# Performance work log

Hardware: AMD Instinct MI355X
Metric: run time of the kernel (lower is better)

The kernel has to match this reference:

```python
import jax, jax.numpy as jnp
import numpy as np

BINS = 10

def setup_inputs() -> dict:
    key = jax.random.key(0)
    k1, k2 = jax.random.split(key)
    N, C = 262144, 80
    pred = jax.random.normal(k1, (N, C), dtype=jnp.float32)
    target = jax.random.randint(k2, (N, C), 0, 2, dtype=jnp.int32)
    return {"pred": pred, "target": target}


def _ghmc_loss(pred, target):
    # NOTE: faithful to the original torch code, which applies sigmoid to pred
    # and then feeds that *through binary_cross_entropy_with_logits* (i.e. the
    # sigmoid output is treated as logits -- a double sigmoid quirk we preserve).
    z = jax.nn.sigmoid(pred)                      # [N, C] "logits" fed to BCE-with-logits
    t = target.astype(z.dtype)                    # [N, C]
    # gradient magnitude, detached like pred.detach() in torch
    g = jnp.abs(jax.lax.stop_gradient(z) - t)     # in [0, 1]
    # label_weight is overwritten with ones in the original forward, so every
    # element is valid: tot = N * C.
    tot = jnp.asarray(z.size, dtype=z.dtype)

    # uniform bins: edges[i] = i/BINS, last edge nudged by 1e-6 so g == 1 lands
    # in the last bin -> equivalent to floor(g*BINS) clipped to BINS-1.
    idx = jnp.clip((g * BINS).astype(jnp.int32), 0, BINS - 1)   # [N, C]
    counts = jax.ops.segment_sum(
        jnp.ones((z.size,), dtype=z.dtype), idx.reshape(-1), num_segments=BINS
    )                                                            # [BINS]
    n_nonempty = jnp.sum(counts > 0).astype(z.dtype)
    per_bin_w = jnp.where(counts > 0, tot / jnp.maximum(counts, 1.0), 0.0)  # [BINS]
    weights = per_bin_w[idx] / jnp.maximum(n_nonempty, 1.0)      # [N, C]
    weights = jax.lax.stop_gradient(weights)

    # BCE-with-logits(z, t) = softplus(z) - t*z (numerically stable)
    bce = jax.nn.softplus(z) - t * z
    return jnp.sum(weights * bce) / tot


def reference(pred, target):
    return _ghmc_loss(pred, target)
```

## Files before the change

kernel.cpp:

```cpp
#include <hip/hip_runtime.h>


#define NBINS  10
#define GRID1  2048
#define BLOCK1 256

typedef float vf4 __attribute__((ext_vector_type(4)));
typedef int   vi4 __attribute__((ext_vector_type(4)));

#if __has_builtin(__builtin_amdgcn_exp2f)
__device__ __forceinline__ float nexp2(float a) { return __builtin_amdgcn_exp2f(a); }
#else
__device__ __forceinline__ float nexp2(float a) { return __expf(a * 0.69314718055994531f); }
#endif
#if __has_builtin(__builtin_amdgcn_logf)
__device__ __forceinline__ float nlog2(float a) { return __builtin_amdgcn_logf(a); }
#else
__device__ __forceinline__ float nlog2(float a) { return __logf(a) * 1.44269504088896341f; }
#endif

#define LOG2E 1.44269504088896341f
#define LN2   0.69314718055994531f

__global__ __launch_bounds__(BLOCK1) void ghmc_pass1(
    const vf4* __restrict__ pred4,
    const vi4* __restrict__ targ4,
    float* __restrict__ partial_s,
    int*   __restrict__ partial_c,
    int nvec4)
{
    __shared__ float sred[BLOCK1 / 64][NBINS];
    __shared__ int   cred[BLOCK1 / 64][NBINS];

    float s[NBINS];
#pragma unroll
    for (int b = 0; b < NBINS; ++b) s[b] = 0.0f;
    unsigned long long cnt = 0;

    const int idx    = blockIdx.x * BLOCK1 + threadIdx.x;
    const int stride = GRID1 * BLOCK1;

    auto group8 = [&](vf4 p0, vi4 t0, vf4 p1, vi4 t1) {
        float x[8], tf[8];
#pragma unroll
        for (int j = 0; j < 4; ++j) {
            x[j]     = p0[j];  tf[j]     = (float)t0[j];
            x[4 + j] = p1[j];  tf[4 + j] = (float)t1[j];
        }
        float z[8];
#pragma unroll
        for (int j = 0; j < 8; ++j)
            z[j] = __builtin_amdgcn_rcpf(1.0f + nexp2(-x[j] * LOG2E));
        asm volatile("" : "+v"(z[0]), "+v"(z[1]), "+v"(z[2]), "+v"(z[3]),
                         "+v"(z[4]), "+v"(z[5]), "+v"(z[6]), "+v"(z[7]));
        int bi[8]; float bce[8];
#pragma unroll
        for (int j = 0; j < 8; ++j) {
            float g = fabsf(z[j] - tf[j]);
            int   b = (int)(g * 10.0f);
            bi[j]   = b > (NBINS - 1) ? (NBINS - 1) : b;
            float sp = nlog2(1.0f + nexp2(z[j] * LOG2E)) * LN2;
            bce[j]  = sp - tf[j] * z[j];
        }
#pragma unroll
        for (int j = 0; j < 8; ++j) {
#pragma unroll
            for (int b = 0; b < NBINS; ++b)
                s[b] += (bi[j] == b) ? bce[j] : 0.0f;
            cnt += 1ull << (6 * bi[j]);
        }
    };

    int i = idx;
    for (; i + 3 * stride < nvec4; i += 4 * stride) {
        vf4 p0 = pred4[i];
        vi4 t0 = targ4[i];
        vf4 p1 = pred4[i + stride];
        vi4 t1 = targ4[i + stride];
        vf4 p2 = pred4[i + 2 * stride];
        vi4 t2 = targ4[i + 2 * stride];
        vf4 p3 = pred4[i + 3 * stride];
        vi4 t3 = targ4[i + 3 * stride];
        asm volatile("" : "+v"(p0), "+v"(t0), "+v"(p1), "+v"(t1),
                          "+v"(p2), "+v"(t2), "+v"(p3), "+v"(t3));
        group8(p0, t0, p1, t1);
        group8(p2, t2, p3, t3);
    }
    for (; i + stride < nvec4; i += 2 * stride) {
        vf4 p0 = pred4[i];
        vi4 t0 = targ4[i];
        vf4 p1 = pred4[i + stride];
        vi4 t1 = targ4[i + stride];
        asm volatile("" : "+v"(p0), "+v"(t0), "+v"(p1), "+v"(t1));
        group8(p0, t0, p1, t1);
    }
    if (i < nvec4) {
        vf4 p0 = pred4[i];
        vi4 t0 = targ4[i];
#pragma unroll
        for (int j = 0; j < 4; ++j) {
            float tfj = (float)t0[j];
            float zj  = __builtin_amdgcn_rcpf(1.0f + nexp2(-p0[j] * LOG2E));
            float g   = fabsf(zj - tfj);
            int   b   = (int)(g * 10.0f);
            b = b > (NBINS - 1) ? (NBINS - 1) : b;
            float bc  = nlog2(1.0f + nexp2(zj * LOG2E)) * LN2 - tfj * zj;
#pragma unroll
            for (int bb = 0; bb < NBINS; ++bb)
                s[bb] += (b == bb) ? bc : 0.0f;
            cnt += 1ull << (6 * b);
        }
    }

    int c[NBINS];
#pragma unroll
    for (int b = 0; b < NBINS; ++b) c[b] = (int)((cnt >> (6 * b)) & 63ull);

#pragma unroll
    for (int b = 0; b < NBINS; ++b) {
#pragma unroll
        for (int off = 32; off > 0; off >>= 1) {
            s[b] += __shfl_down(s[b], off, 64);
            c[b] += __shfl_down(c[b], off, 64);
        }
    }

    const int wave = threadIdx.x >> 6;
    if ((threadIdx.x & 63) == 0) {
#pragma unroll
        for (int b = 0; b < NBINS; ++b) { sred[wave][b] = s[b]; cred[wave][b] = c[b]; }
    }
    __syncthreads();
    if (threadIdx.x < NBINS) {
        int b = threadIdx.x;
        partial_s[b * GRID1 + blockIdx.x] = sred[0][b] + sred[1][b] + sred[2][b] + sred[3][b];
        partial_c[b * GRID1 + blockIdx.x] = cred[0][b] + cred[1][b] + cred[2][b] + cred[3][b];
    }
}

#define BLOCK2 1024

__global__ __launch_bounds__(BLOCK2) void ghmc_pass2(
    const float* __restrict__ partial_s,
    const int*   __restrict__ partial_c,
    float* __restrict__ out,
    int nblocks)
{
    double as[NBINS];
    int    ac[NBINS];
#pragma unroll
    for (int b = 0; b < NBINS; ++b) { as[b] = 0.0; ac[b] = 0; }

    for (int j = threadIdx.x; j < nblocks; j += BLOCK2) {
#pragma unroll
        for (int b = 0; b < NBINS; ++b) {
            as[b] += (double)partial_s[b * nblocks + j];
            ac[b] += partial_c[b * nblocks + j];
        }
    }

#pragma unroll
    for (int b = 0; b < NBINS; ++b) {
#pragma unroll
        for (int off = 32; off > 0; off >>= 1) {
            as[b] += __shfl_down(as[b], off, 64);
            ac[b] += __shfl_down(ac[b], off, 64);
        }
    }

    __shared__ double sds[BLOCK2 / 64][NBINS];
    __shared__ int    sdc[BLOCK2 / 64][NBINS];
    int wave = threadIdx.x >> 6;
    if ((threadIdx.x & 63) == 0) {
#pragma unroll
        for (int b = 0; b < NBINS; ++b) { sds[wave][b] = as[b]; sdc[wave][b] = ac[b]; }
    }
    __syncthreads();

    if (threadIdx.x == 0) {
        int nn = 0;
        double acc = 0.0;
#pragma unroll
        for (int b = 0; b < NBINS; ++b) {
            double sb = 0.0;
            int    cb = 0;
#pragma unroll
            for (int w = 0; w < BLOCK2 / 64; ++w) { sb += sds[w][b]; cb += sdc[w][b]; }
            if (cb > 0) { nn += 1; acc += sb / (double)cb; }
        }
        out[0] = (float)(acc / (double)(nn > 0 ? nn : 1));
    }
}

extern "C" void kernel_launch(void* const* d_in, const int* in_sizes, int n_in,
                              void* d_out, int out_size, void* d_ws, size_t ws_size,
                              hipStream_t stream)
{
    const float* pred = (const float*)d_in[0];
    const int*   targ = (const int*)d_in[1];
    float*       out  = (float*)d_out;

    const int n     = in_sizes[0];
    const int nvec4 = n / 4;

    float* partial_s = (float*)d_ws;
    int*   partial_c = (int*)((char*)d_ws + GRID1 * NBINS * sizeof(float));

    ghmc_pass1<<<GRID1, BLOCK1, 0, stream>>>(
        (const vf4*)pred, (const vi4*)targ, partial_s, partial_c, nvec4);

    ghmc_pass2<<<1, BLOCK2, 0, stream>>>(partial_s, partial_c, out, GRID1);
}
```

Before: 199.9 us.

## Use contiguous per-block chunks with XCD-aware block swizzle and full unroll

When the input size matches the grid exactly, each block reads one contiguous chunk of vec4 elements, fully unrolled, instead of walking a grid-stride loop. Block indices are remapped so that blocks landing on the same XCD cover neighbouring memory regions. Removing the asm register barriers gives the compiler more scheduling freedom. The goal is more loads in flight and better cache/DRAM locality; the fast path is specialized to one exact size, with a generic fallback for other sizes.

```diff
diff --git a/kernel.cpp b/kernel.cpp
--- a/kernel.cpp
+++ b/kernel.cpp
@@ -4,6 +4,7 @@
 #define NBINS  10
 #define GRID1  2048
 #define BLOCK1 256
+#define NXCD   8
 
 typedef float vf4 __attribute__((ext_vector_type(4)));
 typedef int   vi4 __attribute__((ext_vector_type(4)));
@@ -22,6 +23,9 @@
 #define LOG2E 1.44269504088896341f
 #define LN2   0.69314718055994531f
 
+#define VPT   10
+#define CHUNK (VPT * BLOCK1)
+
 __global__ __launch_bounds__(BLOCK1) void ghmc_pass1(
     const vf4* __restrict__ pred4,
     const vi4* __restrict__ targ4,
@@ -37,8 +41,7 @@
     for (int b = 0; b < NBINS; ++b) s[b] = 0.0f;
     unsigned long long cnt = 0;
 
-    const int idx    = blockIdx.x * BLOCK1 + threadIdx.x;
-    const int stride = GRID1 * BLOCK1;
+    const int tid = threadIdx.x;
 
     auto group8 = [&](vf4 p0, vi4 t0, vf4 p1, vi4 t1) {
         float x[8], tf[8];
@@ -51,8 +54,6 @@
 #pragma unroll
         for (int j = 0; j < 8; ++j)
             z[j] = __builtin_amdgcn_rcpf(1.0f + nexp2(-x[j] * LOG2E));
-        asm volatile("" : "+v"(z[0]), "+v"(z[1]), "+v"(z[2]), "+v"(z[3]),
-                         "+v"(z[4]), "+v"(z[5]), "+v"(z[6]), "+v"(z[7]));
         int bi[8]; float bce[8];
 #pragma unroll
         for (int j = 0; j < 8; ++j) {
@@ -71,44 +72,46 @@
         }
     };
 
-    int i = idx;
-    for (; i + 3 * stride < nvec4; i += 4 * stride) {
-        vf4 p0 = pred4[i];
-        vi4 t0 = targ4[i];
-        vf4 p1 = pred4[i + stride];
-        vi4 t1 = targ4[i + stride];
-        vf4 p2 = pred4[i + 2 * stride];
-        vi4 t2 = targ4[i + 2 * stride];
-        vf4 p3 = pred4[i + 3 * stride];
-        vi4 t3 = targ4[i + 3 * stride];
-        asm volatile("" : "+v"(p0), "+v"(t0), "+v"(p1), "+v"(t1),
-                          "+v"(p2), "+v"(t2), "+v"(p3), "+v"(t3));
-        group8(p0, t0, p1, t1);
-        group8(p2, t2, p3, t3);
-    }
-    for (; i + stride < nvec4; i += 2 * stride) {
-        vf4 p0 = pred4[i];
-        vi4 t0 = targ4[i];
-        vf4 p1 = pred4[i + stride];
-        vi4 t1 = targ4[i + stride];
-        asm volatile("" : "+v"(p0), "+v"(t0), "+v"(p1), "+v"(t1));
-        group8(p0, t0, p1, t1);
-    }
-    if (i < nvec4) {
-        vf4 p0 = pred4[i];
-        vi4 t0 = targ4[i];
-#pragma unroll
-        for (int j = 0; j < 4; ++j) {
-            float tfj = (float)t0[j];
-            float zj  = __builtin_amdgcn_rcpf(1.0f + nexp2(-p0[j] * LOG2E));
-            float g   = fabsf(zj - tfj);
-            int   b   = (int)(g * 10.0f);
-            b = b > (NBINS - 1) ? (NBINS - 1) : b;
-            float bc  = nlog2(1.0f + nexp2(zj * LOG2E)) * LN2 - tfj * zj;
-#pragma unroll
-            for (int bb = 0; bb < NBINS; ++bb)
-                s[bb] += (b == bb) ? bc : 0.0f;
-            cnt += 1ull << (6 * b);
+    if (nvec4 == GRID1 * CHUNK) {
+        const int swz  = (blockIdx.x % NXCD) * (GRID1 / NXCD) + blockIdx.x / NXCD;
+        const int base = swz * CHUNK + tid;
+#pragma unroll
+        for (int k = 0; k < VPT; k += 2) {
+            const int i0 = base + k * BLOCK1;
+            const int i1 = i0 + BLOCK1;
+            vf4 p0 = pred4[i0];
+            vi4 t0 = targ4[i0];
+            vf4 p1 = pred4[i1];
+            vi4 t1 = targ4[i1];
+            group8(p0, t0, p1, t1);
+        }
+    } else {
+        const int idx    = blockIdx.x * BLOCK1 + tid;
+        const int stride = GRID1 * BLOCK1;
+        int i = idx;
+        for (; i + stride < nvec4; i += 2 * stride) {
+            vf4 p0 = pred4[i];
+            vi4 t0 = targ4[i];
+            vf4 p1 = pred4[i + stride];
+            vi4 t1 = targ4[i + stride];
+            group8(p0, t0, p1, t1);
+        }
+        if (i < nvec4) {
+            vf4 p0 = pred4[i];
+            vi4 t0 = targ4[i];
+#pragma unroll
+            for (int j = 0; j < 4; ++j) {
+                float tfj = (float)t0[j];
+                float zj  = __builtin_amdgcn_rcpf(1.0f + nexp2(-p0[j] * LOG2E));
+                float g   = fabsf(zj - tfj);
+                int   b   = (int)(g * 10.0f);
+                b = b > (NBINS - 1) ? (NBINS - 1) : b;
+                float bc  = nlog2(1.0f + nexp2(zj * LOG2E)) * LN2 - tfj * zj;
+#pragma unroll
+                for (int bb = 0; bb < NBINS; ++bb)
+                    s[bb] += (b == bb) ? bc : 0.0f;
+                cnt += 1ull << (6 * b);
+            }
         }
     }
 
@@ -125,14 +128,14 @@
         }
     }
 
-    const int wave = threadIdx.x >> 6;
-    if ((threadIdx.x & 63) == 0) {
+    const int wave = tid >> 6;
+    if ((tid & 63) == 0) {
 #pragma unroll
         for (int b = 0; b < NBINS; ++b) { sred[wave][b] = s[b]; cred[wave][b] = c[b]; }
     }
     __syncthreads();
-    if (threadIdx.x < NBINS) {
-        int b = threadIdx.x;
+    if (tid < NBINS) {
+        int b = tid;
         partial_s[b * GRID1 + blockIdx.x] = sred[0][b] + sred[1][b] + sred[2][b] + sred[3][b];
         partial_c[b * GRID1 + blockIdx.x] = cred[0][b] + cred[1][b] + cred[2][b] + cred[3][b];
     }
```

Measured after the change: 203.0 us. Within noise of the previous version (+1.6%).
